# Kernel optimization log

Measured on AMD Instinct MI355X. Metric: run time of the kernel, lower is better.

## Reference

```python
import jax, jax.numpy as jnp
import numpy as np

# 8-neighbor offsets matching compute_rd ordering:
# top, bottom, left, right, left_top, right_top, left_bottom, right_bottom
_DY = jnp.array([-1, 1, 0, 0, -1, -1, 1, 1], dtype=jnp.int32)
_DX = jnp.array([0, 0, -1, 1, -1, 1, -1, 1], dtype=jnp.int32)


def _rd(depth, px, py):
    # depth: [B,1,H,W]; px,py: [P] -> returns [B,P,8] relative-depth diffs
    d = depth[:, 0]                                    # [B,H,W]
    center = d[:, py, px]                              # [B,P]
    nbr = d[:, py[:, None] + _DY[None, :], px[:, None] + _DX[None, :]]  # [B,P,8]
    return center[:, :, None] - nbr


def _normalize_rows(v):
    # L2 norm over last dim; rows with zero norm divided by 1.0 (masked_fill)
    n = jnp.linalg.norm(v, axis=-1, keepdims=True)
    n = jnp.where(n == 0, jnp.ones_like(n), n)
    return v / n


def setup_inputs() -> dict:
    key = jax.random.key(0)
    k1, k2 = jax.random.split(key)
    B, H, W, P = 64, 384, 384, 1000
    pred = jax.random.normal(k1, (B, 1, H, W), dtype=jnp.float32)
    gt = jax.random.normal(k2, (B, 1, H, W), dtype=jnp.float32)
    rng = np.random.RandomState(0)
    px = jnp.asarray(rng.randint(30, 350, size=P), dtype=jnp.int32)
    py = jnp.asarray(rng.randint(30, 350, size=P), dtype=jnp.int32)
    return {"pred": pred, "gt": gt, "px": px, "py": py}


def reference(pred, gt, px, py):
    p = _normalize_rows(_rd(pred, px, py))
    g = _normalize_rows(_rd(gt, px, py))
    return jnp.mean(jnp.abs(p - g))
```

## Files before the change

### kernel.cpp

```cpp
#include <hip/hip_runtime.h>

#define BB 64
#define HH 384
#define WW 384
#define PP 1000
#define NITEMS (BB * PP)
#define NTERMS (NITEMS * 8)

__global__ __launch_bounds__(256)
void rd_loss_kernel(const float* __restrict__ pred,
                    const float* __restrict__ gt,
                    const int*   __restrict__ px,
                    const int*   __restrict__ py,
                    float* __restrict__ out) {
    const int idx = blockIdx.x * blockDim.x + threadIdx.x;
    float partial = 0.0f;
    if (idx < NITEMS) {
        const int b = idx / PP;
        const int p = idx - b * PP;
        const int x = px[p];
        const int y = py[p];
        const float* pb = pred + (size_t)b * (HH * WW);
        const float* gb = gt   + (size_t)b * (HH * WW);
        const int c = y * WW + x;
        const float pc = pb[c];
        const float gc = gb[c];
        const int off[8] = { c - WW, c + WW, c - 1, c + 1,
                             c - WW - 1, c - WW + 1, c + WW - 1, c + WW + 1 };
        float vp[8], vg[8];
        float sp = 0.0f, sg = 0.0f;
        #pragma unroll
        for (int i = 0; i < 8; ++i) {
            vp[i] = pc - pb[off[i]];
            vg[i] = gc - gb[off[i]];
            sp += vp[i] * vp[i];
            sg += vg[i] * vg[i];
        }
        float npn = sqrtf(sp); if (npn == 0.0f) npn = 1.0f;
        float ngn = sqrtf(sg); if (ngn == 0.0f) ngn = 1.0f;
        const float ip = 1.0f / npn;
        const float ig = 1.0f / ngn;
        float s = 0.0f;
        #pragma unroll
        for (int i = 0; i < 8; ++i)
            s += fabsf(vp[i] * ip - vg[i] * ig);
        partial = s;
    }

    #pragma unroll
    for (int o = 32; o > 0; o >>= 1)
        partial += __shfl_down(partial, o, 64);

    __shared__ float wsum[4];
    const int lane = threadIdx.x & 63;
    const int wid  = threadIdx.x >> 6;
    if (lane == 0) wsum[wid] = partial;
    __syncthreads();
    if (threadIdx.x == 0) {
        float t = wsum[0] + wsum[1] + wsum[2] + wsum[3];
        atomicAdd(out, t * (1.0f / (float)NTERMS));
    }
}

extern "C" void kernel_launch(void* const* d_in, const int* in_sizes, int n_in,
                              void* d_out, int out_size, void* d_ws, size_t ws_size,
                              hipStream_t stream) {
    const float* pred = (const float*)d_in[0];
    const float* gt   = (const float*)d_in[1];
    const int*   px   = (const int*)d_in[2];
    const int*   py   = (const int*)d_in[3];
    float* out = (float*)d_out;

    hipMemsetAsync(out, 0, sizeof(float), stream);

    const int block = 256;
    const int grid = (NITEMS + block - 1) / block;
    rd_loss_kernel<<<grid, block, 0, stream>>>(pred, gt, px, py, out);
}
```

Baseline: 103.4 us.

## Assign one thread per neighbor and reduce row norms with lane shuffles

The kernel now uses eight threads per (batch, point) item, each loading one neighbor. The squared norms are combined across the 8-lane group with xor shuffles, and rsqrt replaces sqrt plus divide. The aim is more memory-level parallelism and better latency hiding for the scattered gathers. The cost is eight times as many threads and atomics, redundant center and px/py loads, and extra shuffle work.

```diff
diff --git a/kernel.cpp b/kernel.cpp
--- a/kernel.cpp
+++ b/kernel.cpp
@@ -5,7 +5,11 @@
 #define WW 384
 #define PP 1000
 #define NITEMS (BB * PP)
+#define NTHREADS (NITEMS * 8)
 #define NTERMS (NITEMS * 8)
+
+#define DYC 0xA058
+#define DXC 0x8885
 
 __global__ __launch_bounds__(256)
 void rd_loss_kernel(const float* __restrict__ pred,
@@ -13,43 +17,49 @@
                     const int*   __restrict__ px,
                     const int*   __restrict__ py,
                     float* __restrict__ out) {
-    const int idx = blockIdx.x * blockDim.x + threadIdx.x;
-    float partial = 0.0f;
-    if (idx < NITEMS) {
-        const int b = idx / PP;
-        const int p = idx - b * PP;
-        const int x = px[p];
-        const int y = py[p];
-        const float* pb = pred + (size_t)b * (HH * WW);
-        const float* gb = gt   + (size_t)b * (HH * WW);
-        const int c = y * WW + x;
-        const float pc = pb[c];
-        const float gc = gb[c];
-        const int off[8] = { c - WW, c + WW, c - 1, c + 1,
-                             c - WW - 1, c - WW + 1, c + WW - 1, c + WW + 1 };
-        float vp[8], vg[8];
-        float sp = 0.0f, sg = 0.0f;
-        #pragma unroll
-        for (int i = 0; i < 8; ++i) {
-            vp[i] = pc - pb[off[i]];
-            vg[i] = gc - gb[off[i]];
-            sp += vp[i] * vp[i];
-            sg += vg[i] * vg[i];
-        }
-        float npn = sqrtf(sp); if (npn == 0.0f) npn = 1.0f;
-        float ngn = sqrtf(sg); if (ngn == 0.0f) ngn = 1.0f;
-        const float ip = 1.0f / npn;
-        const float ig = 1.0f / ngn;
-        float s = 0.0f;
-        #pragma unroll
-        for (int i = 0; i < 8; ++i)
-            s += fabsf(vp[i] * ip - vg[i] * ig);
-        partial = s;
-    }
+    const int t = blockIdx.x * 256 + threadIdx.x;
+    const int item = t >> 3;
+    const int i    = t & 7;
 
-    #pragma unroll
-    for (int o = 32; o > 0; o >>= 1)
-        partial += __shfl_down(partial, o, 64);
+    const int b = item / PP;
+    const int p = item - b * PP;
+    const int x = px[p];
+    const int y = py[p];
+
+    const float* pb = pred + (size_t)b * (HH * WW);
+    const float* gb = gt   + (size_t)b * (HH * WW);
+    const int c = y * WW + x;
+
+    const int i2 = i << 1;
+    const int dy = ((DYC >> i2) & 3) - 1;
+    const int dx = ((DXC >> i2) & 3) - 1;
+    const int off = c + dy * WW + dx;
+
+    const float pc = pb[c];
+    const float gc = gb[c];
+    const float vp = pc - pb[off];
+    const float vg = gc - gb[off];
+
+    float sp = vp * vp;
+    float sg = vg * vg;
+    sp += __shfl_xor(sp, 1, 64);
+    sp += __shfl_xor(sp, 2, 64);
+    sp += __shfl_xor(sp, 4, 64);
+    sg += __shfl_xor(sg, 1, 64);
+    sg += __shfl_xor(sg, 2, 64);
+    sg += __shfl_xor(sg, 4, 64);
+
+    const float ip = (sp == 0.0f) ? 1.0f : rsqrtf(sp);
+    const float ig = (sg == 0.0f) ? 1.0f : rsqrtf(sg);
+
+    float partial = fabsf(vp * ip - vg * ig);
+
+    partial += __shfl_xor(partial, 1, 64);
+    partial += __shfl_xor(partial, 2, 64);
+    partial += __shfl_xor(partial, 4, 64);
+    partial += __shfl_xor(partial, 8, 64);
+    partial += __shfl_xor(partial, 16, 64);
+    partial += __shfl_xor(partial, 32, 64);
 
     __shared__ float wsum[4];
     const int lane = threadIdx.x & 63;
@@ -57,8 +67,8 @@
     if (lane == 0) wsum[wid] = partial;
     __syncthreads();
     if (threadIdx.x == 0) {
-        float t = wsum[0] + wsum[1] + wsum[2] + wsum[3];
-        atomicAdd(out, t * (1.0f / (float)NTERMS));
+        const float tsum = wsum[0] + wsum[1] + wsum[2] + wsum[3];
+        atomicAdd(out, tsum * (1.0f / (float)NTERMS));
     }
 }
 
@@ -74,6 +84,6 @@
     hipMemsetAsync(out, 0, sizeof(float), stream);
 
     const int block = 256;
-    const int grid = (NITEMS + block - 1) / block;
+    const int grid = NTHREADS / block;
     rd_loss_kernel<<<grid, block, 0, stream>>>(pred, gt, px, py, out);
 }
```

After: 123.1 us. 1.19x slower.

## Load 3x3 neighborhoods as float3 rows and replace atomics with two-stage reduction

Applied to the files above, without the earlier changes.

Each pixel's 3x3 neighborhood is now read as three 12-byte row loads per image instead of nine scalar loads. The single atomicAdd reduction, which needed a memset, is replaced by per-block partials in workspace plus a one-block second-stage kernel. rsqrt replaces sqrt and divide, and the bounds check is dropped because 64000 items divide evenly into 250 blocks. The aim is fewer memory instructions and no memset or atomic serialization, at the cost of an extra kernel launch and a dependence on workspace being available.

```diff
diff --git a/kernel.cpp b/kernel.cpp
--- a/kernel.cpp
+++ b/kernel.cpp
@@ -6,46 +6,52 @@
 #define PP 1000
 #define NITEMS (BB * PP)
 #define NTERMS (NITEMS * 8)
+#define NBLOCKS1 250
+
+struct __attribute__((aligned(4))) F3 { float a, b, c; };
 
 __global__ __launch_bounds__(256)
-void rd_loss_kernel(const float* __restrict__ pred,
-                    const float* __restrict__ gt,
-                    const int*   __restrict__ px,
-                    const int*   __restrict__ py,
-                    float* __restrict__ out) {
-    const int idx = blockIdx.x * blockDim.x + threadIdx.x;
+void rd_stage1(const float* __restrict__ pred,
+               const float* __restrict__ gt,
+               const int*   __restrict__ px,
+               const int*   __restrict__ py,
+               float* __restrict__ partials) {
+    const int idx = blockIdx.x * 256 + threadIdx.x;
+    const int b = idx / PP;
+    const int p = idx - b * PP;
+    const int x = px[p];
+    const int y = py[p];
+
+    const float* pb = pred + (size_t)b * (HH * WW);
+    const float* gb = gt   + (size_t)b * (HH * WW);
+    const int c = y * WW + x;
+
+    const F3 pt = *(const F3*)(pb + c - WW - 1);
+    const F3 pm = *(const F3*)(pb + c      - 1);
+    const F3 pbo= *(const F3*)(pb + c + WW - 1);
+    const F3 gt_= *(const F3*)(gb + c - WW - 1);
+    const F3 gm = *(const F3*)(gb + c      - 1);
+    const F3 gbo= *(const F3*)(gb + c + WW - 1);
+
+    const float pc = pm.b, gc = gm.b;
+    const float pn[8] = { pt.b, pbo.b, pm.a, pm.c, pt.a, pt.c, pbo.a, pbo.c };
+    const float gn[8] = { gt_.b, gbo.b, gm.a, gm.c, gt_.a, gt_.c, gbo.a, gbo.c };
+
+    float vp[8], vg[8], sp = 0.0f, sg = 0.0f;
+    #pragma unroll
+    for (int i = 0; i < 8; ++i) {
+        vp[i] = pc - pn[i];
+        vg[i] = gc - gn[i];
+        sp += vp[i] * vp[i];
+        sg += vg[i] * vg[i];
+    }
+    const float ip = (sp == 0.0f) ? 1.0f : rsqrtf(sp);
+    const float ig = (sg == 0.0f) ? 1.0f : rsqrtf(sg);
+
     float partial = 0.0f;
-    if (idx < NITEMS) {
-        const int b = idx / PP;
-        const int p = idx - b * PP;
-        const int x = px[p];
-        const int y = py[p];
-        const float* pb = pred + (size_t)b * (HH * WW);
-        const float* gb = gt   + (size_t)b * (HH * WW);
-        const int c = y * WW + x;
-        const float pc = pb[c];
-        const float gc = gb[c];
-        const int off[8] = { c - WW, c + WW, c - 1, c + 1,
-                             c - WW - 1, c - WW + 1, c + WW - 1, c + WW + 1 };
-        float vp[8], vg[8];
-        float sp = 0.0f, sg = 0.0f;
-        #pragma unroll
-        for (int i = 0; i < 8; ++i) {
-            vp[i] = pc - pb[off[i]];
-            vg[i] = gc - gb[off[i]];
-            sp += vp[i] * vp[i];
-            sg += vg[i] * vg[i];
-        }
-        float npn = sqrtf(sp); if (npn == 0.0f) npn = 1.0f;
-        float ngn = sqrtf(sg); if (ngn == 0.0f) ngn = 1.0f;
-        const float ip = 1.0f / npn;
-        const float ig = 1.0f / ngn;
-        float s = 0.0f;
-        #pragma unroll
-        for (int i = 0; i < 8; ++i)
-            s += fabsf(vp[i] * ip - vg[i] * ig);
-        partial = s;
-    }
+    #pragma unroll
+    for (int i = 0; i < 8; ++i)
+        partial += fabsf(vp[i] * ip - vg[i] * ig);
 
     #pragma unroll
     for (int o = 32; o > 0; o >>= 1)
@@ -56,10 +62,24 @@
     const int wid  = threadIdx.x >> 6;
     if (lane == 0) wsum[wid] = partial;
     __syncthreads();
-    if (threadIdx.x == 0) {
-        float t = wsum[0] + wsum[1] + wsum[2] + wsum[3];
-        atomicAdd(out, t * (1.0f / (float)NTERMS));
-    }
+    if (threadIdx.x == 0)
+        partials[blockIdx.x] = wsum[0] + wsum[1] + wsum[2] + wsum[3];
+}
+
+__global__ __launch_bounds__(256)
+void rd_stage2(const float* __restrict__ partials, float* __restrict__ out) {
+    const int t = threadIdx.x;
+    float v = (t < NBLOCKS1) ? partials[t] : 0.0f;
+    #pragma unroll
+    for (int o = 32; o > 0; o >>= 1)
+        v += __shfl_down(v, o, 64);
+
+    __shared__ float wsum[4];
+    const int lane = t & 63, wid = t >> 6;
+    if (lane == 0) wsum[wid] = v;
+    __syncthreads();
+    if (t == 0)
+        out[0] = (wsum[0] + wsum[1] + wsum[2] + wsum[3]) * (1.0f / (float)NTERMS);
 }
 
 extern "C" void kernel_launch(void* const* d_in, const int* in_sizes, int n_in,
@@ -69,11 +89,9 @@
     const float* gt   = (const float*)d_in[1];
     const int*   px   = (const int*)d_in[2];
     const int*   py   = (const int*)d_in[3];
-    float* out = (float*)d_out;
+    float* out      = (float*)d_out;
+    float* partials = (float*)d_ws;
 
-    hipMemsetAsync(out, 0, sizeof(float), stream);
-
-    const int block = 256;
-    const int grid = (NITEMS + block - 1) / block;
-    rd_loss_kernel<<<grid, block, 0, stream>>>(pred, gt, px, py, out);
+    rd_stage1<<<NBLOCKS1, 256, 0, stream>>>(pred, gt, px, py, partials);
+    rd_stage2<<<1, 256, 0, stream>>>(partials, out);
 }
```

After: 101.5 us. No clear change (-1.9%).
